# Kernel optimization log

Hardware: AMD Instinct MI355X
Metric: run time of the kernel (lower is better)

Reference implementation:

```python
import jax, jax.numpy as jnp
import numpy as np

NH = 12  # num_heads

def setup_inputs() -> dict:
    key = jax.random.key(0)
    ks = jax.random.split(key, 8)
    B, N, C = 8, 1024, 768
    d = C // NH  # head_dim == qk_head_dim (qk_head_dim=None)
    s = 0.02
    return {
        "x": jax.random.normal(ks[0], (B, N, C), jnp.float32),
        "Wq": jax.random.normal(ks[1], (C, NH * d), jnp.float32) * s,
        "Wk": jax.random.normal(ks[2], (C, NH * d), jnp.float32) * s,
        "Wv": jax.random.normal(ks[3], (C, C), jnp.float32) * s,
        "Wproj": jax.random.normal(ks[4], (C, C), jnp.float32) * s,
        "proj_b": jax.random.normal(ks[5], (C,), jnp.float32) * s,
        "attn_bias": jax.random.normal(ks[6], (N, N), jnp.float32) * s,
        "head_bias": jax.random.normal(ks[7], (NH, N, N), jnp.float32) * s,
    }

def reference(x, Wq, Wk, Wv, Wproj, proj_b, attn_bias, head_bias):
    B, N, C = x.shape
    d = C // NH
    scale = d ** -0.5
    # projections: [B,N,C] -> [B,nh,N,d]
    q = jnp.einsum('bnc,ce->bne', x, Wq).reshape(B, N, NH, d).transpose(0, 2, 1, 3)
    k = jnp.einsum('bnc,ce->bne', x, Wk).reshape(B, N, NH, d).transpose(0, 2, 1, 3)
    v = jnp.einsum('bnc,ce->bne', x, Wv).reshape(B, N, NH, d).transpose(0, 2, 1, 3)
    # scaled scores + global bias + per-head bias
    scores = jnp.einsum('bhnd,bhmd->bhnm', q * scale, k)
    scores = scores + attn_bias[None, None] + head_bias[None]
    attn = jax.nn.softmax(scores, axis=-1)  # [B,nh,N,N]
    out = jnp.einsum('bhnm,bhmd->bhnd', attn, v)
    out = out.transpose(0, 2, 1, 3).reshape(B, N, C)
    out = jnp.einsum('bnc,ce->bne', out, Wproj) + proj_b
    return out, attn
```

## Files before the change

kernel.cpp:

```cpp
#include <hip/hip_runtime.h>
#include <hip/hip_bf16.h>
#include <cstddef>

#define B_   8
#define N_   1024
#define C_   768
#define NH_  12
#define HD_  64
#define M_   (B_ * N_)

typedef __attribute__((ext_vector_type(8))) short  short8;
typedef __attribute__((ext_vector_type(4))) float  f32x4;

__device__ __forceinline__ unsigned short f2b(float f) {
    union { float f; unsigned u; } v; v.f = f;
    unsigned u = v.u;
    return (unsigned short)((u + 0x7FFFu + ((u >> 16) & 1u)) >> 16);
}
__device__ __forceinline__ float b2f(unsigned short s) {
    union { unsigned u; float f; } v; v.u = ((unsigned)s) << 16;
    return v.f;
}
__device__ __forceinline__ ushort2 pk2(float a, float b) {
    __hip_bfloat162 t = __float22bfloat162_rn(make_float2(a, b));
    return *(ushort2*)&t;
}
__device__ __forceinline__ void gld16(const unsigned short* g, unsigned short* l) {
    __builtin_amdgcn_global_load_lds(
        (const __attribute__((address_space(1))) void*)g,
        (__attribute__((address_space(3))) void*)l, 16, 0, 0);
}

__global__ __launch_bounds__(256) void cast_x_kernel(const float* __restrict__ x,
                                                     unsigned short* __restrict__ xb) {
    const int n4 = M_ * C_ / 4;
    for (int i = blockIdx.x * blockDim.x + threadIdx.x; i < n4; i += gridDim.x * blockDim.x) {
        float4 v = ((const float4*)x)[i];
        ushort2 lo = pk2(v.x, v.y), hi = pk2(v.z, v.w);
        ushort4 o; o.x = lo.x; o.y = lo.y; o.z = hi.x; o.w = hi.y;
        ((ushort4*)xb)[i] = o;
    }
}

__global__ __launch_bounds__(256) void bias_combine_kernel(
    const float* __restrict__ ab, const float* __restrict__ hbias,
    unsigned short* __restrict__ bc) {
    const int total4 = NH_ * N_ * N_ / 4;
    const int qm4 = N_ * N_ / 4;
    for (int i = blockIdx.x * blockDim.x + threadIdx.x; i < total4; i += gridDim.x * blockDim.x) {
        int rem = i % qm4;
        float4 a = ((const float4*)ab)[rem];
        float4 h = ((const float4*)hbias)[i];
        ushort2 lo = pk2(a.x + h.x, a.y + h.y), hi = pk2(a.z + h.z, a.w + h.w);
        ushort4 o; o.x = lo.x; o.y = lo.y; o.z = hi.x; o.w = hi.y;
        ((ushort4*)bc)[i] = o;
    }
}

__global__ __launch_bounds__(256) void transpose_cast_kernel(
    const float* __restrict__ w0, const float* __restrict__ w1,
    const float* __restrict__ w2, const float* __restrict__ w3,
    unsigned short* __restrict__ t0, unsigned short* __restrict__ t1,
    unsigned short* __restrict__ t2, unsigned short* __restrict__ t3) {
    const int z = blockIdx.z;
    const float* src = (z == 0) ? w0 : (z == 1) ? w1 : (z == 2) ? w2 : w3;
    unsigned short* dst = (z == 0) ? t0 : (z == 1) ? t1 : (z == 2) ? t2 : t3;
    __shared__ float tile[32][33];
    const int r0 = blockIdx.y * 32, c0 = blockIdx.x * 32;
    const int tx = threadIdx.x & 31, ty = threadIdx.x >> 5;
    #pragma unroll
    for (int p = 0; p < 4; ++p)
        tile[ty + 8 * p][tx] = src[(size_t)(r0 + ty + 8 * p) * C_ + c0 + tx];
    __syncthreads();
    #pragma unroll
    for (int p = 0; p < 4; ++p)
        dst[(size_t)(c0 + ty + 8 * p) * C_ + r0 + tx] = f2b(tile[tx][ty + 8 * p]);
}

__global__ __launch_bounds__(256) void qkv_gemm(
    const unsigned short* __restrict__ A,
    const unsigned short* __restrict__ W0, const unsigned short* __restrict__ W1,
    const unsigned short* __restrict__ W2,
    unsigned short* __restrict__ o0, unsigned short* __restrict__ o1,
    unsigned short* __restrict__ o2) {
    __shared__ unsigned short As[128 * 32];
    __shared__ unsigned short Bs[128 * 32];
    const int z = blockIdx.z;
    const unsigned short* Bt = (z == 0) ? W0 : (z == 1) ? W1 : W2;
    const int tid = threadIdx.x;
    const int wid = tid >> 6, lane = tid & 63;
    const int ln = lane & 15, g = lane >> 4;
    const int wm = wid >> 1, wn = wid & 1;
    const int bm = blockIdx.y * 128, bn = blockIdx.x * 128;
    const int lrow = lane >> 2, lch = (lane & 3) * 8;

    f32x4 acc[4][4];
    #pragma unroll
    for (int i = 0; i < 4; ++i)
        #pragma unroll
        for (int j = 0; j < 4; ++j) acc[i][j] = (f32x4)0.f;

    for (int k0 = 0; k0 < C_; k0 += 32) {
        #pragma unroll
        for (int p = 0; p < 2; ++p) {
            const int rowbase = (wid + p * 4) * 16;
            gld16(&A [(size_t)(bm + rowbase + lrow) * C_ + k0 + lch], &As[rowbase * 32]);
            gld16(&Bt[(size_t)(bn + rowbase + lrow) * C_ + k0 + lch], &Bs[rowbase * 32]);
        }
        __syncthreads();
        short8 a[4], b[4];
        #pragma unroll
        for (int mt = 0; mt < 4; ++mt)
            a[mt] = *(const short8*)&As[(wm * 64 + mt * 16 + ln) * 32 + g * 8];
        #pragma unroll
        for (int nt = 0; nt < 4; ++nt)
            b[nt] = *(const short8*)&Bs[(wn * 64 + nt * 16 + ln) * 32 + g * 8];
        #pragma unroll
        for (int mt = 0; mt < 4; ++mt)
            #pragma unroll
            for (int nt = 0; nt < 4; ++nt)
                acc[mt][nt] = __builtin_amdgcn_mfma_f32_16x16x32_bf16(
                    a[mt], b[nt], acc[mt][nt], 0, 0, 0);
        __syncthreads();
    }

    unsigned short* outp = (z == 0) ? o0 : (z == 1) ? o1 : o2;
    #pragma unroll
    for (int mt = 0; mt < 4; ++mt) {
        #pragma unroll
        for (int nt = 0; nt < 4; ++nt) {
            f32x4 c = acc[mt][nt];
            int rowb = bm + wm * 64 + mt * 16 + g * 4;
            int col  = bn + wn * 64 + nt * 16 + ln;
            int hh = col >> 6, dd = col & 63;
            if (z < 2) {
                #pragma unroll
                for (int i = 0; i < 4; ++i) {
                    int row = rowb + i;
                    int bb = row >> 10, n = row & 1023;
                    outp[((size_t)(bb * NH_ + hh) * N_ + n) * HD_ + dd] = f2b(c[i]);
                }
            } else {
                int bb = rowb >> 10, n0 = rowb & 1023;
                ushort2 lo = pk2(c[0], c[1]), hi = pk2(c[2], c[3]);
                ushort4 pk; pk.x = lo.x; pk.y = lo.y; pk.z = hi.x; pk.w = hi.y;
                *(ushort4*)&outp[((size_t)(bb * NH_ + hh) * HD_ + dd) * N_ + n0] = pk;
            }
        }
    }
}

__global__ __launch_bounds__(256) void proj_gemm(
    const unsigned short* __restrict__ A, const unsigned short* __restrict__ Bt,
    const float* __restrict__ bias, float* __restrict__ outp) {
    __shared__ unsigned short As[128 * 32];
    __shared__ unsigned short Bs[128 * 32];
    const int tid = threadIdx.x;
    const int wid = tid >> 6, lane = tid & 63;
    const int ln = lane & 15, g = lane >> 4;
    const int wm = wid >> 1, wn = wid & 1;
    const int bm = blockIdx.y * 128, bn = blockIdx.x * 128;
    const int lrow = lane >> 2, lch = (lane & 3) * 8;

    f32x4 acc[4][4];
    #pragma unroll
    for (int i = 0; i < 4; ++i)
        #pragma unroll
        for (int j = 0; j < 4; ++j) acc[i][j] = (f32x4)0.f;

    for (int k0 = 0; k0 < C_; k0 += 32) {
        #pragma unroll
        for (int p = 0; p < 2; ++p) {
            const int rowbase = (wid + p * 4) * 16;
            gld16(&A [(size_t)(bm + rowbase + lrow) * C_ + k0 + lch], &As[rowbase * 32]);
            gld16(&Bt[(size_t)(bn + rowbase + lrow) * C_ + k0 + lch], &Bs[rowbase * 32]);
        }
        __syncthreads();
        short8 a[4], b[4];
        #pragma unroll
        for (int mt = 0; mt < 4; ++mt)
            a[mt] = *(const short8*)&As[(wm * 64 + mt * 16 + ln) * 32 + g * 8];
        #pragma unroll
        for (int nt = 0; nt < 4; ++nt)
            b[nt] = *(const short8*)&Bs[(wn * 64 + nt * 16 + ln) * 32 + g * 8];
        #pragma unroll
        for (int mt = 0; mt < 4; ++mt)
            #pragma unroll
            for (int nt = 0; nt < 4; ++nt)
                acc[mt][nt] = __builtin_amdgcn_mfma_f32_16x16x32_bf16(
                    a[mt], b[nt], acc[mt][nt], 0, 0, 0);
        __syncthreads();
    }

    #pragma unroll
    for (int mt = 0; mt < 4; ++mt) {
        #pragma unroll
        for (int nt = 0; nt < 4; ++nt) {
            f32x4 c = acc[mt][nt];
            int rowb = bm + wm * 64 + mt * 16 + g * 4;
            int col  = bn + wn * 64 + nt * 16 + ln;
            float bb = bias[col];
            #pragma unroll
            for (int i = 0; i < 4; ++i)
                outp[(size_t)(rowb + i) * C_ + col] = c[i] + bb;
        }
    }
}

__global__ __launch_bounds__(512, 4) void attn_fused(
    const unsigned short* __restrict__ qh, const unsigned short* __restrict__ kh,
    const unsigned short* __restrict__ vt,
    const unsigned short* __restrict__ bias_c,
    float* __restrict__ attn_out, unsigned short* __restrict__ hb) {
    __shared__ unsigned short sc[32 * 1024];
    __shared__ float sinv[32];
    const int id = blockIdx.x;
    const int xcd = id & 7;
    const int b = (id >> 3) & 7;
    const int qbh = ((id >> 6) << 3) + xcd;
    const int qb0 = (qbh / NH_) * 32;
    const int h = qbh % NH_;
    const int bh = b * NH_ + h;
    const int tid = threadIdx.x;
    const int wid = tid >> 6, lane = tid & 63;
    const int ln = lane & 15, g = lane >> 4;

    #define SCP(row, m) ((unsigned short*)((char*)sc + (row) * 2048 + \
                         (((m) * 2) ^ (((row) & 7) << 4))))

    {
        short8 qf[2][2];
        #pragma unroll
        for (int Mt = 0; Mt < 2; ++Mt)
            #pragma unroll
            for (int kc = 0; kc < 2; ++kc)
                qf[Mt][kc] = *(const short8*)&qh[
                    ((size_t)bh * N_ + qb0 + Mt * 16 + ln) * HD_ + kc * 32 + g * 8];
        const int mb = wid * 128;
        const unsigned short* kbase = kh + (size_t)bh * N_ * HD_;
        short8 k0 = *(const short8*)&kbase[(size_t)(mb + ln) * HD_ + g * 8];
        short8 k1 = *(const short8*)&kbase[(size_t)(mb + ln) * HD_ + 32 + g * 8];
        for (int mt = 0; mt < 8; ++mt) {
            const int m0 = mb + mt * 16;
            const int m1 = (mt < 7) ? m0 + 16 : m0;
            short8 n0 = *(const short8*)&kbase[(size_t)(m1 + ln) * HD_ + g * 8];
            short8 n1 = *(const short8*)&kbase[(size_t)(m1 + ln) * HD_ + 32 + g * 8];
            #pragma unroll
            for (int Mt = 0; Mt < 2; ++Mt) {
                f32x4 s = (f32x4)0.f;
                s = __builtin_amdgcn_mfma_f32_16x16x32_bf16(k0, qf[Mt][0], s, 0, 0, 0);
                s = __builtin_amdgcn_mfma_f32_16x16x32_bf16(k1, qf[Mt][1], s, 0, 0, 0);
                const int mrow = m0 + g * 4;
                ushort2 lo = pk2(s[0] * 0.125f, s[1] * 0.125f);
                ushort2 hi = pk2(s[2] * 0.125f, s[3] * 0.125f);
                ushort4 pk; pk.x = lo.x; pk.y = lo.y; pk.z = hi.x; pk.w = hi.y;
                *(ushort4*)SCP(Mt * 16 + ln, mrow) = pk;
            }
            k0 = n0; k1 = n1;
        }
    }
    __syncthreads();

    f32x4 sv[16];
    const int r2 = tid >> 4, t16 = tid & 15;
    {
        const unsigned short* brow = bias_c + ((size_t)h * N_ + qb0 + r2) * N_;
        float mx = -1e30f;
        #pragma unroll
        for (int j = 0; j < 16; ++j) {
            ushort4 er = *(const ushort4*)SCP(r2, t16 * 4 + j * 64);
            ushort4 bb = *(const ushort4*)&brow[t16 * 4 + j * 64];
            sv[j][0] = b2f(er.x) + b2f(bb.x);
            sv[j][1] = b2f(er.y) + b2f(bb.y);
            sv[j][2] = b2f(er.z) + b2f(bb.z);
            sv[j][3] = b2f(er.w) + b2f(bb.w);
            mx = fmaxf(fmaxf(fmaxf(mx, sv[j][0]), fmaxf(sv[j][1], sv[j][2])), sv[j][3]);
        }
        #pragma unroll
        for (int off = 8; off; off >>= 1) mx = fmaxf(mx, __shfl_xor(mx, off, 16));
        float sum = 0.f;
        #pragma unroll
        for (int j = 0; j < 16; ++j) {
            float e0 = __expf(sv[j][0] - mx);
            float e1 = __expf(sv[j][1] - mx);
            float e2 = __expf(sv[j][2] - mx);
            float e3 = __expf(sv[j][3] - mx);
            sv[j][0] = e0; sv[j][1] = e1; sv[j][2] = e2; sv[j][3] = e3;
            sum += (e0 + e1) + (e2 + e3);
            ushort2 lo = pk2(e0, e1), hi = pk2(e2, e3);
            ushort4 pk; pk.x = lo.x; pk.y = lo.y; pk.z = hi.x; pk.w = hi.y;
            *(ushort4*)SCP(r2, t16 * 4 + j * 64) = pk;
        }
        #pragma unroll
        for (int off = 8; off; off >>= 1) sum += __shfl_xor(sum, off, 16);
        if (t16 == 0) sinv[r2] = 1.f / sum;
    }
    __syncthreads();

    {
        const float invr = sinv[r2];
        float* arow = attn_out + ((size_t)bh * N_ + qb0 + r2) * N_ + t16 * 4;
        const int Mt = wid >> 2, nt = wid & 3;
        const unsigned short* vrow = vt + ((size_t)bh * HD_ + nt * 16 + ln) * N_;
        f32x4 acc = (f32x4)0.f;
        short8 pa = *(const short8*)SCP(Mt * 16 + ln, g * 8);
        short8 vb = *(const short8*)&vrow[g * 8];
        #pragma unroll
        for (int kt2 = 0; kt2 < 16; ++kt2) {
            {
                const int kn = 2 * kt2 + 1;
                short8 npa = *(const short8*)SCP(Mt * 16 + ln, kn * 32 + g * 8);
                short8 nvb = *(const short8*)&vrow[kn * 32 + g * 8];
                acc = __builtin_amdgcn_mfma_f32_16x16x32_bf16(pa, vb, acc, 0, 0, 0);
                pa = npa; vb = nvb;
            }
            {
                f32x4 o;
                o[0] = sv[kt2][0] * invr; o[1] = sv[kt2][1] * invr;
                o[2] = sv[kt2][2] * invr; o[3] = sv[kt2][3] * invr;
                __builtin_nontemporal_store(o, (f32x4*)&arow[kt2 * 64]);
            }
            {
                const int kn = (kt2 < 15) ? 2 * kt2 + 2 : 2 * kt2 + 1;
                short8 npa = *(const short8*)SCP(Mt * 16 + ln, kn * 32 + g * 8);
                short8 nvb = *(const short8*)&vrow[kn * 32 + g * 8];
                acc = __builtin_amdgcn_mfma_f32_16x16x32_bf16(pa, vb, acc, 0, 0, 0);
                pa = npa; vb = nvb;
            }
        }
        #pragma unroll
        for (int i = 0; i < 4; ++i) {
            int q = qb0 + Mt * 16 + g * 4 + i;
            float o = acc[i] * sinv[Mt * 16 + g * 4 + i];
            hb[(size_t)((b << 10) + q) * C_ + h * HD_ + nt * 16 + ln] = f2b(o);
        }
    }
    #undef SCP
}

extern "C" void kernel_launch(void* const* d_in, const int* in_sizes, int n_in,
                              void* d_out, int out_size, void* d_ws, size_t ws_size,
                              hipStream_t stream) {
    const float* x         = (const float*)d_in[0];
    const float* Wq        = (const float*)d_in[1];
    const float* Wk        = (const float*)d_in[2];
    const float* Wv        = (const float*)d_in[3];
    const float* Wproj     = (const float*)d_in[4];
    const float* proj_b    = (const float*)d_in[5];
    const float* attn_bias = (const float*)d_in[6];
    const float* head_bias = (const float*)d_in[7];

    float* out  = (float*)d_out;
    float* attn = out + (size_t)B_ * N_ * C_;

    unsigned short* ws = (unsigned short*)d_ws;
    const size_t SZ_X = (size_t)M_ * C_;
    const size_t SZ_W = (size_t)C_ * C_;
    unsigned short* xb  = ws;
    unsigned short* wqt = xb + SZ_X;
    unsigned short* wkt = wqt + SZ_W;
    unsigned short* wvt = wkt + SZ_W;
    unsigned short* wpt = wvt + SZ_W;
    unsigned short* qh  = wpt + SZ_W;
    unsigned short* khd = qh + SZ_X;
    unsigned short* vtp = khd + SZ_X;
    unsigned short* bc  = vtp + SZ_X;
    unsigned short* hb  = xb;

    cast_x_kernel<<<2048, 256, 0, stream>>>(x, xb);
    bias_combine_kernel<<<2048, 256, 0, stream>>>(attn_bias, head_bias, bc);
    transpose_cast_kernel<<<dim3(24, 24, 4), 256, 0, stream>>>(
        Wq, Wk, Wv, Wproj, wqt, wkt, wvt, wpt);

    qkv_gemm<<<dim3(C_ / 128, M_ / 128, 3), 256, 0, stream>>>(
        xb, wqt, wkt, wvt, qh, khd, vtp);

    attn_fused<<<dim3(B_ * (N_ / 32) * NH_), 512, 0, stream>>>(
        qh, khd, vtp, bc, attn, hb);

    proj_gemm<<<dim3(C_ / 128, M_ / 128), 256, 0, stream>>>(hb, wpt, proj_b, out);
}
```

Measured before the change: 293.6 us.

## Merge prepass kernels into one launch and double GEMM K-tile to 64

Fuses the x cast, bias combine and weight transpose-cast kernels into a single launch that splits blocks by role, removing two launches and the gaps between them. Both GEMMs now stage a 64-wide K slice per iteration and run two MFMA sub-steps per tile, which halves the number of barrier pairs per K loop. The price is twice the LDS per block, which may reduce occupancy, and a 64-element row stride in LDS that can raise bank conflicts.

```diff
diff --git a/kernel.cpp b/kernel.cpp
--- a/kernel.cpp
+++ b/kernel.cpp
@@ -31,50 +31,51 @@
         (__attribute__((address_space(3))) void*)l, 16, 0, 0);
 }
 
-__global__ __launch_bounds__(256) void cast_x_kernel(const float* __restrict__ x,
-                                                     unsigned short* __restrict__ xb) {
-    const int n4 = M_ * C_ / 4;
-    for (int i = blockIdx.x * blockDim.x + threadIdx.x; i < n4; i += gridDim.x * blockDim.x) {
-        float4 v = ((const float4*)x)[i];
-        ushort2 lo = pk2(v.x, v.y), hi = pk2(v.z, v.w);
-        ushort4 o; o.x = lo.x; o.y = lo.y; o.z = hi.x; o.w = hi.y;
-        ((ushort4*)xb)[i] = o;
-    }
-}
-
-__global__ __launch_bounds__(256) void bias_combine_kernel(
-    const float* __restrict__ ab, const float* __restrict__ hbias,
-    unsigned short* __restrict__ bc) {
-    const int total4 = NH_ * N_ * N_ / 4;
-    const int qm4 = N_ * N_ / 4;
-    for (int i = blockIdx.x * blockDim.x + threadIdx.x; i < total4; i += gridDim.x * blockDim.x) {
-        int rem = i % qm4;
-        float4 a = ((const float4*)ab)[rem];
-        float4 h = ((const float4*)hbias)[i];
-        ushort2 lo = pk2(a.x + h.x, a.y + h.y), hi = pk2(a.z + h.z, a.w + h.w);
-        ushort4 o; o.x = lo.x; o.y = lo.y; o.z = hi.x; o.w = hi.y;
-        ((ushort4*)bc)[i] = o;
-    }
-}
-
-__global__ __launch_bounds__(256) void transpose_cast_kernel(
+__global__ __launch_bounds__(256) void prepass_kernel(
+    const float* __restrict__ x,
     const float* __restrict__ w0, const float* __restrict__ w1,
     const float* __restrict__ w2, const float* __restrict__ w3,
+    const float* __restrict__ ab, const float* __restrict__ hbias,
+    unsigned short* __restrict__ xb,
     unsigned short* __restrict__ t0, unsigned short* __restrict__ t1,
-    unsigned short* __restrict__ t2, unsigned short* __restrict__ t3) {
-    const int z = blockIdx.z;
-    const float* src = (z == 0) ? w0 : (z == 1) ? w1 : (z == 2) ? w2 : w3;
-    unsigned short* dst = (z == 0) ? t0 : (z == 1) ? t1 : (z == 2) ? t2 : t3;
-    __shared__ float tile[32][33];
-    const int r0 = blockIdx.y * 32, c0 = blockIdx.x * 32;
-    const int tx = threadIdx.x & 31, ty = threadIdx.x >> 5;
-    #pragma unroll
-    for (int p = 0; p < 4; ++p)
-        tile[ty + 8 * p][tx] = src[(size_t)(r0 + ty + 8 * p) * C_ + c0 + tx];
-    __syncthreads();
-    #pragma unroll
-    for (int p = 0; p < 4; ++p)
-        dst[(size_t)(c0 + ty + 8 * p) * C_ + r0 + tx] = f2b(tile[tx][ty + 8 * p]);
+    unsigned short* __restrict__ t2, unsigned short* __restrict__ t3,
+    unsigned short* __restrict__ bc) {
+    const int bid = blockIdx.x;
+    if (bid < 2304) {
+        const int z = bid / 576, t = bid % 576;
+        const float* src = (z == 0) ? w0 : (z == 1) ? w1 : (z == 2) ? w2 : w3;
+        unsigned short* dst = (z == 0) ? t0 : (z == 1) ? t1 : (z == 2) ? t2 : t3;
+        __shared__ float tile[32][33];
+        const int r0 = (t / 24) * 32, c0 = (t % 24) * 32;
+        const int tx = threadIdx.x & 31, ty = threadIdx.x >> 5;
+        #pragma unroll
+        for (int p = 0; p < 4; ++p)
+            tile[ty + 8 * p][tx] = src[(size_t)(r0 + ty + 8 * p) * C_ + c0 + tx];
+        __syncthreads();
+        #pragma unroll
+        for (int p = 0; p < 4; ++p)
+            dst[(size_t)(c0 + ty + 8 * p) * C_ + r0 + tx] = f2b(tile[tx][ty + 8 * p]);
+    } else {
+        const int castN4 = M_ * C_ / 4;
+        const int biasN4 = NH_ * N_ * N_ / 4;
+        const int qm4 = N_ * N_ / 4;
+        const int stride = (4096 - 2304) * 256;
+        for (int i = (bid - 2304) * 256 + threadIdx.x; i < castN4 + biasN4; i += stride) {
+            if (i < castN4) {
+                float4 v = ((const float4*)x)[i];
+                ushort2 lo = pk2(v.x, v.y), hi = pk2(v.z, v.w);
+                ushort4 o; o.x = lo.x; o.y = lo.y; o.z = hi.x; o.w = hi.y;
+                ((ushort4*)xb)[i] = o;
+            } else {
+                int j = i - castN4;
+                float4 a = ((const float4*)ab)[j % qm4];
+                float4 h = ((const float4*)hbias)[j];
+                ushort2 lo = pk2(a.x + h.x, a.y + h.y), hi = pk2(a.z + h.z, a.w + h.w);
+                ushort4 o; o.x = lo.x; o.y = lo.y; o.z = hi.x; o.w = hi.y;
+                ((ushort4*)bc)[j] = o;
+            }
+        }
+    }
 }
 
 __global__ __launch_bounds__(256) void qkv_gemm(
@@ -83,8 +84,8 @@
     const unsigned short* __restrict__ W2,
     unsigned short* __restrict__ o0, unsigned short* __restrict__ o1,
     unsigned short* __restrict__ o2) {
-    __shared__ unsigned short As[128 * 32];
-    __shared__ unsigned short Bs[128 * 32];
+    __shared__ unsigned short As[128 * 64];
+    __shared__ unsigned short Bs[128 * 64];
     const int z = blockIdx.z;
     const unsigned short* Bt = (z == 0) ? W0 : (z == 1) ? W1 : W2;
     const int tid = threadIdx.x;
@@ -92,7 +93,7 @@
     const int ln = lane & 15, g = lane >> 4;
     const int wm = wid >> 1, wn = wid & 1;
     const int bm = blockIdx.y * 128, bn = blockIdx.x * 128;
-    const int lrow = lane >> 2, lch = (lane & 3) * 8;
+    const int lrow = lane >> 3, lch = (lane & 7) * 8;
 
     f32x4 acc[4][4];
     #pragma unroll
@@ -100,27 +101,30 @@
         #pragma unroll
         for (int j = 0; j < 4; ++j) acc[i][j] = (f32x4)0.f;
 
-    for (int k0 = 0; k0 < C_; k0 += 32) {
-        #pragma unroll
-        for (int p = 0; p < 2; ++p) {
-            const int rowbase = (wid + p * 4) * 16;
-            gld16(&A [(size_t)(bm + rowbase + lrow) * C_ + k0 + lch], &As[rowbase * 32]);
-            gld16(&Bt[(size_t)(bn + rowbase + lrow) * C_ + k0 + lch], &Bs[rowbase * 32]);
-        }
-        __syncthreads();
-        short8 a[4], b[4];
-        #pragma unroll
-        for (int mt = 0; mt < 4; ++mt)
-            a[mt] = *(const short8*)&As[(wm * 64 + mt * 16 + ln) * 32 + g * 8];
-        #pragma unroll
-        for (int nt = 0; nt < 4; ++nt)
-            b[nt] = *(const short8*)&Bs[(wn * 64 + nt * 16 + ln) * 32 + g * 8];
-        #pragma unroll
-        for (int mt = 0; mt < 4; ++mt)
+    for (int k0 = 0; k0 < C_; k0 += 64) {
+        #pragma unroll
+        for (int p = 0; p < 4; ++p) {
+            const int rowbase = wid * 32 + p * 8;
+            gld16(&A [(size_t)(bm + rowbase + lrow) * C_ + k0 + lch], &As[rowbase * 64]);
+            gld16(&Bt[(size_t)(bn + rowbase + lrow) * C_ + k0 + lch], &Bs[rowbase * 64]);
+        }
+        __syncthreads();
+        #pragma unroll
+        for (int kk = 0; kk < 2; ++kk) {
+            short8 a[4], b[4];
+            #pragma unroll
+            for (int mt = 0; mt < 4; ++mt)
+                a[mt] = *(const short8*)&As[(wm * 64 + mt * 16 + ln) * 64 + kk * 32 + g * 8];
             #pragma unroll
             for (int nt = 0; nt < 4; ++nt)
-                acc[mt][nt] = __builtin_amdgcn_mfma_f32_16x16x32_bf16(
-                    a[mt], b[nt], acc[mt][nt], 0, 0, 0);
+                b[nt] = *(const short8*)&Bs[(wn * 64 + nt * 16 + ln) * 64 + kk * 32 + g * 8];
+            #pragma unroll
+            for (int mt = 0; mt < 4; ++mt)
+                #pragma unroll
+                for (int nt = 0; nt < 4; ++nt)
+                    acc[mt][nt] = __builtin_amdgcn_mfma_f32_16x16x32_bf16(
+                        a[mt], b[nt], acc[mt][nt], 0, 0, 0);
+        }
         __syncthreads();
     }
 
@@ -153,14 +157,14 @@
 __global__ __launch_bounds__(256) void proj_gemm(
     const unsigned short* __restrict__ A, const unsigned short* __restrict__ Bt,
     const float* __restrict__ bias, float* __restrict__ outp) {
-    __shared__ unsigned short As[128 * 32];
-    __shared__ unsigned short Bs[128 * 32];
+    __shared__ unsigned short As[128 * 64];
+    __shared__ unsigned short Bs[128 * 64];
     const int tid = threadIdx.x;
     const int wid = tid >> 6, lane = tid & 63;
     const int ln = lane & 15, g = lane >> 4;
     const int wm = wid >> 1, wn = wid & 1;
     const int bm = blockIdx.y * 128, bn = blockIdx.x * 128;
-    const int lrow = lane >> 2, lch = (lane & 3) * 8;
+    const int lrow = lane >> 3, lch = (lane & 7) * 8;
 
     f32x4 acc[4][4];
     #pragma unroll
@@ -168,27 +172,30 @@
         #pragma unroll
         for (int j = 0; j < 4; ++j) acc[i][j] = (f32x4)0.f;
 
-    for (int k0 = 0; k0 < C_; k0 += 32) {
-        #pragma unroll
-        for (int p = 0; p < 2; ++p) {
-            const int rowbase = (wid + p * 4) * 16;
-            gld16(&A [(size_t)(bm + rowbase + lrow) * C_ + k0 + lch], &As[rowbase * 32]);
-            gld16(&Bt[(size_t)(bn + rowbase + lrow) * C_ + k0 + lch], &Bs[rowbase * 32]);
-        }
-        __syncthreads();
-        short8 a[4], b[4];
-        #pragma unroll
-        for (int mt = 0; mt < 4; ++mt)
-            a[mt] = *(const short8*)&As[(wm * 64 + mt * 16 + ln) * 32 + g * 8];
-        #pragma unroll
-        for (int nt = 0; nt < 4; ++nt)
-            b[nt] = *(const short8*)&Bs[(wn * 64 + nt * 16 + ln) * 32 + g * 8];
-        #pragma unroll
-        for (int mt = 0; mt < 4; ++mt)
+    for (int k0 = 0; k0 < C_; k0 += 64) {
+        #pragma unroll
+        for (int p = 0; p < 4; ++p) {
+            const int rowbase = wid * 32 + p * 8;
+            gld16(&A [(size_t)(bm + rowbase + lrow) * C_ + k0 + lch], &As[rowbase * 64]);
+            gld16(&Bt[(size_t)(bn + rowbase + lrow) * C_ + k0 + lch], &Bs[rowbase * 64]);
+        }
+        __syncthreads();
+        #pragma unroll
+        for (int kk = 0; kk < 2; ++kk) {
+            short8 a[4], b[4];
+            #pragma unroll
+            for (int mt = 0; mt < 4; ++mt)
+                a[mt] = *(const short8*)&As[(wm * 64 + mt * 16 + ln) * 64 + kk * 32 + g * 8];
             #pragma unroll
             for (int nt = 0; nt < 4; ++nt)
-                acc[mt][nt] = __builtin_amdgcn_mfma_f32_16x16x32_bf16(
-                    a[mt], b[nt], acc[mt][nt], 0, 0, 0);
+                b[nt] = *(const short8*)&Bs[(wn * 64 + nt * 16 + ln) * 64 + kk * 32 + g * 8];
+            #pragma unroll
+            for (int mt = 0; mt < 4; ++mt)
+                #pragma unroll
+                for (int nt = 0; nt < 4; ++nt)
+                    acc[mt][nt] = __builtin_amdgcn_mfma_f32_16x16x32_bf16(
+                        a[mt], b[nt], acc[mt][nt], 0, 0, 0);
+        }
         __syncthreads();
     }
 
@@ -367,10 +374,9 @@
     unsigned short* bc  = vtp + SZ_X;
     unsigned short* hb  = xb;
 
-    cast_x_kernel<<<2048, 256, 0, stream>>>(x, xb);
-    bias_combine_kernel<<<2048, 256, 0, stream>>>(attn_bias, head_bias, bc);
-    transpose_cast_kernel<<<dim3(24, 24, 4), 256, 0, stream>>>(
-        Wq, Wk, Wv, Wproj, wqt, wkt, wvt, wpt);
+    prepass_kernel<<<4096, 256, 0, stream>>>(
+        x, Wq, Wk, Wv, Wproj, attn_bias, head_bias,
+        xb, wqt, wkt, wvt, wpt, bc);
 
     qkv_gemm<<<dim3(C_ / 128, M_ / 128, 3), 256, 0, stream>>>(
         xb, wqt, wkt, wvt, qh, khd, vtp);
```

New measurement: 298.5 us. No clear change (+1.7%).
